# Kernel optimization log

Hardware: AMD Instinct MI355X
Metric: run time of the kernel (lower is better)

## Reference

```python
import jax, jax.numpy as jnp
import numpy as np

RADIUS = 4        # config.corr_radius
NUM_LEVELS = 4    # config.corr_levels
EPS = 1e-12       # F.normalize eps


def _avg_pool(x, s):
    # F.avg_pool2d(x, s, stride=s) for H,W divisible by s
    if s == 1:
        return x
    B, C, H, W = x.shape
    return x.reshape(B, C, H // s, s, W // s, s).mean(axis=(3, 5))


def _l2_normalize(x):
    # F.normalize(x, dim=1): x / max(||x||_2, eps)
    n = jnp.sqrt(jnp.sum(x * x, axis=1, keepdims=True))
    return x / jnp.maximum(n, EPS)


def _correlation(f1, f2, r=RADIUS):
    # windowed local correlation: corr[dy,dx](y,x) = sum_c f1(y,x) * f2(y-dy, x-dx)
    B, C, H, W = f1.shape
    f1 = _l2_normalize(f1)
    f2 = _l2_normalize(f2)
    f2p = jnp.pad(f2, ((0, 0), (0, 0), (r, r), (r, r)))  # zero pad = zero fill outside
    corrs = []
    for dy in range(-r, r + 1):
        for dx in range(-r, r + 1):
            sh = jax.lax.slice(f2p, (0, 0, r - dy, r - dx), (B, C, r - dy + H, r - dx + W))
            corrs.append(jnp.sum(f1 * sh, axis=1))  # [B,H,W]
    return jnp.stack(corrs, axis=1)  # [B, (2r+1)^2, H, W]


def setup_inputs() -> dict:
    key = jax.random.key(0)
    k1, k2, k3, k4 = jax.random.split(key, 4)
    B, C, H, W = 4, 256, 128, 192
    return {
        "fmap1": jax.random.normal(k1, (B, C, H, W), jnp.float32),
        "fmap2": jax.random.normal(k2, (B, C, H, W), jnp.float32),
        "depth1": jax.random.uniform(k3, (B, 1, H, W), jnp.float32),
        "depth2": jax.random.uniform(k4, (B, 1, H, W), jnp.float32),
        "depth_weight": jnp.asarray(0.1, jnp.float32),
    }


def reference(fmap1, fmap2, depth1, depth2, depth_weight):
    pyramid = []
    for i in range(NUM_LEVELS):
        s = 2 ** i
        corr = _correlation(_avg_pool(fmap1, s), _avg_pool(fmap2, s))
        # depth correlation enhancement: exp(-|d1 - d2|), broadcast over 81 channels
        dd = jnp.abs(_avg_pool(depth1, s) - _avg_pool(depth2, s))  # [B,1,h,w]
        corr = corr + depth_weight * jnp.exp(-dd)
        pyramid.append(corr)
    return tuple(pyramid)
```

## Files before the change

### kernel.cpp

```cpp
#include <hip/hip_runtime.h>
#include <hip/hip_bf16.h>

typedef __attribute__((ext_vector_type(8))) __bf16 bf16x8;
typedef __attribute__((ext_vector_type(4))) float f32x4;
typedef unsigned short ushort_t;
typedef unsigned int uint_t;

#define CCH 256
#define BB 4

#define NP32_0 3145728
#define NP32_1 786432
#define NP32_2 196608
#define NP32_3 49152

__device__ __forceinline__ ushort_t f2b(float v) {
    __hip_bfloat16 h = __float2bfloat16(v);
    return *reinterpret_cast<ushort_t*>(&h);
}

__device__ __forceinline__ void gload16(const void* g, void* l) {
    __builtin_amdgcn_global_load_lds(
        (const __attribute__((address_space(1))) void*)g,
        (__attribute__((address_space(3))) void*)l, 16, 0, 0);
}

struct PrepPtrs {
    ushort_t* o0; ushort_t* o1; ushort_t* o2; ushort_t* o3;
    float* n0; float* n1; float* n2; float* n3;
};

__global__ __launch_bounds__(256, 3) void pyr_prep_kernel(
    const float* __restrict__ fa, const float* __restrict__ fb,
    PrepPtrs Pa, PrepPtrs Pb)
{
    const int H = 128, W = 192;
    const int HW = H * W;
    const float* fin = blockIdx.y ? fb : fa;
    PrepPtrs P = blockIdx.y ? Pb : Pa;

    __shared__ float lds0[32 * 260];
    __shared__ float lds1[32 * 68];
    __shared__ float lds2[32 * 20];
    __shared__ float red[256];

    int xc = blockIdx.x % 6;
    int ys = (blockIdx.x / 6) % 16;
    int b  = blockIdx.x / 96;
    int gx0 = xc * 32, gy0 = ys * 8;
    int t = threadIdx.x;

    const float* gsrc[8];
    int lofs[8];
    #pragma unroll
    for (int j = 0; j < 8; ++j) {
        int e = t + 256 * j;
        int c = e >> 6, r = (e >> 3) & 7, x4 = e & 7;
        gsrc[j] = fin + ((size_t)(b * 256 + c) * H + gy0 + r) * W + gx0 + 4 * x4;
        lofs[j] = c * 260 + r * 32 + 4 * x4;
    }

    float4 stg[8];
    auto issue = [&](int kc) {
        #pragma unroll
        for (int j = 0; j < 8; ++j)
            stg[j] = *reinterpret_cast<const float4*>(gsrc[j] + (size_t)kc * (32 * HW));
    };

    float ssq0 = 0.f, ssq1 = 0.f, ssq2 = 0.f, ssq3 = 0.f;

    size_t p0g = (size_t)(b * H + gy0 + (t >> 5)) * W + gx0 + (t & 31);
    int wv = t >> 6, q = t & 63, qy = q >> 4, qx = q & 15;
    size_t l1g = (size_t)(b * 64 + ys * 4 + qy) * 96 + xc * 16 + qx;
    int cb2 = t >> 4, sI = t & 15, sy2 = sI >> 3, sx2 = sI & 7;
    size_t l2g = (size_t)(b * 32 + ys * 2 + sy2) * 48 + xc * 8 + sx2;
    int cb3 = t >> 2, u3 = t & 3;
    size_t l3g = (size_t)(b * 16 + ys) * 24 + xc * 4 + u3;

    issue(0);
    #pragma unroll 1
    for (int kc = 0; kc < 8; ++kc) {
        #pragma unroll
        for (int j = 0; j < 8; ++j)
            *reinterpret_cast<float4*>(&lds0[lofs[j]]) = stg[j];
        if (kc < 7) issue(kc + 1);
        __syncthreads();

        {
            uint_t uu[16];
            #pragma unroll
            for (int i = 0; i < 16; ++i) {
                float va = lds0[(2 * i) * 260 + t];
                float vb = lds0[(2 * i + 1) * 260 + t];
                ssq0 = fmaf(va, va, ssq0);
                ssq0 = fmaf(vb, vb, ssq0);
                uu[i] = (uint_t)f2b(va) | ((uint_t)f2b(vb) << 16);
            }
            ushort_t* dst = P.o0 + (size_t)kc * NP32_0 + p0g * 32;
            *reinterpret_cast<uint4*>(dst +  0) = make_uint4(uu[0],  uu[1],  uu[2],  uu[3]);
            *reinterpret_cast<uint4*>(dst +  8) = make_uint4(uu[4],  uu[5],  uu[6],  uu[7]);
            *reinterpret_cast<uint4*>(dst + 16) = make_uint4(uu[8],  uu[9],  uu[10], uu[11]);
            *reinterpret_cast<uint4*>(dst + 24) = make_uint4(uu[12], uu[13], uu[14], uu[15]);
        }

        {
            float a8[8];
            #pragma unroll
            for (int h = 0; h < 8; ++h) {
                int c = wv * 8 + h;
                float2 s0 = *reinterpret_cast<const float2*>(&lds0[c * 260 + (2 * qy) * 32 + 2 * qx]);
                float2 s1 = *reinterpret_cast<const float2*>(&lds0[c * 260 + (2 * qy + 1) * 32 + 2 * qx]);
                a8[h] = 0.25f * (s0.x + s0.y + s1.x + s1.y);
                ssq1 = fmaf(a8[h], a8[h], ssq1);
            }
            uint_t vv[4];
            #pragma unroll
            for (int i = 0; i < 4; ++i)
                vv[i] = (uint_t)f2b(a8[2 * i]) | ((uint_t)f2b(a8[2 * i + 1]) << 16);
            *reinterpret_cast<uint4*>(P.o1 + (size_t)kc * NP32_1 + l1g * 32 + wv * 8)
                = make_uint4(vv[0], vv[1], vv[2], vv[3]);
            #pragma unroll
            for (int h = 0; h < 8; ++h)
                lds1[(wv * 8 + h) * 68 + q] = a8[h];
        }
        __syncthreads();

        if (t < 128) {
            float a4[4];
            #pragma unroll
            for (int cc = 0; cc < 4; ++cc) {
                int c = cb2 * 4 + cc;
                float2 s0 = *reinterpret_cast<const float2*>(&lds1[c * 68 + (2 * sy2) * 16 + 2 * sx2]);
                float2 s1 = *reinterpret_cast<const float2*>(&lds1[c * 68 + (2 * sy2 + 1) * 16 + 2 * sx2]);
                a4[cc] = 0.25f * (s0.x + s0.y + s1.x + s1.y);
                ssq2 = fmaf(a4[cc], a4[cc], ssq2);
            }
            uint_t w0 = (uint_t)f2b(a4[0]) | ((uint_t)f2b(a4[1]) << 16);
            uint_t w1 = (uint_t)f2b(a4[2]) | ((uint_t)f2b(a4[3]) << 16);
            *reinterpret_cast<uint2*>(P.o2 + (size_t)kc * NP32_2 + l2g * 32 + cb2 * 4) = make_uint2(w0, w1);
            #pragma unroll
            for (int cc = 0; cc < 4; ++cc)
                lds2[(cb2 * 4 + cc) * 20 + sI] = a4[cc];
        }
        __syncthreads();

        if (t < 32) {
            float a4[4];
            #pragma unroll
            for (int cc = 0; cc < 4; ++cc) {
                int c = cb3 * 4 + cc;
                float2 s0 = *reinterpret_cast<const float2*>(&lds2[c * 20 + 2 * u3]);
                float2 s1 = *reinterpret_cast<const float2*>(&lds2[c * 20 + 8 + 2 * u3]);
                a4[cc] = 0.25f * (s0.x + s0.y + s1.x + s1.y);
                ssq3 = fmaf(a4[cc], a4[cc], ssq3);
            }
            uint_t w0 = (uint_t)f2b(a4[0]) | ((uint_t)f2b(a4[1]) << 16);
            uint_t w1 = (uint_t)f2b(a4[2]) | ((uint_t)f2b(a4[3]) << 16);
            *reinterpret_cast<uint2*>(P.o3 + (size_t)kc * NP32_3 + l3g * 32 + cb3 * 4) = make_uint2(w0, w1);
        }
    }

    P.n0[p0g] = 1.f / fmaxf(sqrtf(ssq0), 1e-12f);
    red[t] = ssq1;
    __syncthreads();
    if (t < 64) {
        float sm = red[t] + red[t + 64] + red[t + 128] + red[t + 192];
        P.n1[(size_t)(b * 64 + ys * 4 + (t >> 4)) * 96 + xc * 16 + (t & 15)]
            = 1.f / fmaxf(sqrtf(sm), 1e-12f);
    }
    __syncthreads();
    if (t < 128) red[t] = ssq2;
    __syncthreads();
    if (t < 16) {
        float sm = 0.f;
        #pragma unroll
        for (int c = 0; c < 8; ++c) sm += red[t + 16 * c];
        P.n2[(size_t)(b * 32 + ys * 2 + (t >> 3)) * 48 + xc * 8 + (t & 7)]
            = 1.f / fmaxf(sqrtf(sm), 1e-12f);
    }
    __syncthreads();
    if (t < 32) red[t] = ssq3;
    __syncthreads();
    if (t < 4) {
        float sm = 0.f;
        #pragma unroll
        for (int c = 0; c < 8; ++c) sm += red[t + 4 * c];
        P.n3[(size_t)(b * 16 + ys) * 24 + xc * 4 + t]
            = 1.f / fmaxf(sqrtf(sm), 1e-12f);
    }
}

struct CorrLvl {
    const ushort_t* f1n; const ushort_t* f2n;
    const float* in1; const float* in2; const float* dt;
    float* out;
    int H, W, TX, TY, npix32;
};

__global__ __launch_bounds__(256, 2) void corr_fused_kernel(
    CorrLvl Lv0, CorrLvl Lv1, CorrLvl Lv2, const ushort_t* __restrict__ zblk)
{
    __shared__ char smem[65536];
    char* As = smem;
    char* Bs = smem + 16384;

    int bid = blockIdx.x;
    CorrLvl L;
    int local;
    if (bid < 768)      { L = Lv0; local = bid; }
    else if (bid < 960) { L = Lv1; local = bid - 768; }
    else                { L = Lv2; local = bid - 960; }

    int H = L.H, W = L.W, TX = L.TX, TY = L.TY, npix32 = L.npix32;
    int cpx = (BB * TX * TY) >> 3;
    int swz = (local & 7) * cpx + (local >> 3);
    int tx = swz % TX;
    int ty = (swz / TX) % TY;
    int b  = swz / (TX * TY);
    int x0 = tx * 16, y0 = ty * 8;

    int tid = threadIdx.x;
    int w = tid >> 6, lane = tid & 63;
    int kg = lane >> 4, col = lane & 15;
    int r2 = col >> 2, c2 = col & 3;
    int sy = w >> 1, p = w & 1;
    int kgx = kg ^ c2;

    const ushort_t* srcA[2]; char* ldsA[2];
    #pragma unroll
    for (int q = 0; q < 2; ++q) {
        int row = w * 2 + q;
        int px = lane >> 2, js = lane & 3;
        int j = js ^ (px & 3);
        srcA[q] = L.f1n + ((size_t)((b * H + y0 + row) * W) + x0 + px) * 32 + j * 8;
        ldsA[q] = As + row * 1024;
    }
    const ushort_t* srcB[6]; int advB[6]; char* ldsB[6];
    #pragma unroll
    for (int q = 0; q < 6; ++q) {
        int u = (w * 6 + q) * 64 + lane;
        int row = u / 96, rem = u % 96;
        int px = rem >> 2, js = rem & 3;
        int j = js ^ (px & 3);
        int py = y0 - 4 + row, pxg = x0 - 4 + px;
        bool v = (py >= 0) && (py < H) && (pxg >= 0) && (pxg < W);
        srcB[q] = v ? (L.f2n + ((size_t)((b * H + py) * W) + pxg) * 32 + j * 8) : (zblk + j * 8);
        advB[q] = v ? npix32 : 0;
        ldsB[q] = Bs + (w * 6 + q) * 1024;
    }

    int aoff[2], boff[3][4];
    #pragma unroll
    for (int s = 0; s < 2; ++s) {
        int ly = 4 * sy + r2;
        int lx = 4 * (2 * p + s) + c2;
        aoff[s] = ((ly * 16 + lx) * 4 + kgx) * 16;
    }
    #pragma unroll
    for (int i = 0; i < 3; ++i)
        #pragma unroll
        for (int j = 0; j < 4; ++j) {
            int wy = 4 * (sy + i) + r2;
            int wx = 4 * (2 * p + j) + c2;
            boff[i][j] = ((wy * 24 + wx) * 4 + kgx) * 16;
        }

    f32x4 acc0[3][3] = {};
    f32x4 acc1[3][3] = {};

    #pragma unroll
    for (int q = 0; q < 2; ++q) { gload16(srcA[q], ldsA[q]); srcA[q] += npix32; }
    #pragma unroll
    for (int q = 0; q < 6; ++q) { gload16(srcB[q], ldsB[q]); srcB[q] += advB[q]; }

    int buf = 0;
    #pragma unroll 1
    for (int kc = 0; kc < 8; ++kc) {
        if (kc < 7) {
            int boA = (buf ^ 1) * 8192;
            int boB = (buf ^ 1) * 24576;
            #pragma unroll
            for (int q = 0; q < 2; ++q) { gload16(srcA[q], ldsA[q] + boA); srcA[q] += npix32; }
            #pragma unroll
            for (int q = 0; q < 6; ++q) { gload16(srcB[q], ldsB[q] + boB); srcB[q] += advB[q]; }
            __builtin_amdgcn_sched_barrier(0);
            asm volatile("s_waitcnt vmcnt(8)" ::: "memory");
        } else {
            __builtin_amdgcn_sched_barrier(0);
            asm volatile("s_waitcnt vmcnt(0)" ::: "memory");
        }
        __builtin_amdgcn_s_barrier();
        __builtin_amdgcn_sched_barrier(0);

        const char* Ab = As + buf * 8192;
        const char* Bb = Bs + buf * 24576;
        bf16x8 av0 = *(const bf16x8*)(Ab + aoff[0]);
        bf16x8 av1 = *(const bf16x8*)(Ab + aoff[1]);
        #pragma unroll
        for (int i = 0; i < 3; ++i) {
            #pragma unroll
            for (int j = 0; j < 4; ++j) {
                bf16x8 bv = *(const bf16x8*)(Bb + boff[i][j]);
                if (j < 3) acc0[i][j]     = __builtin_amdgcn_mfma_f32_16x16x32_bf16(av0, bv, acc0[i][j], 0, 0, 0);
                if (j > 0) acc1[i][j - 1] = __builtin_amdgcn_mfma_f32_16x16x32_bf16(av1, bv, acc1[i][j - 1], 0, 0, 0);
            }
        }
        if (kc < 7) {
            __builtin_amdgcn_sched_barrier(0);
            __builtin_amdgcn_s_barrier();
            __builtin_amdgcn_sched_barrier(0);
        }
        buf ^= 1;
    }

    float inv1v[2][4], dtv[2][4];
    #pragma unroll
    for (int s = 0; s < 2; ++s) {
        int sxs = 2 * p + s;
        #pragma unroll
        for (int rr = 0; rr < 4; ++rr) {
            int m = kg * 4 + rr;
            int iy = m >> 2, ix = m & 3;
            int pix = (b * H + y0 + 4 * sy + iy) * W + x0 + 4 * sxs + ix;
            inv1v[s][rr] = L.in1[pix];
            dtv[s][rr]   = L.dt[pix];
        }
    }
    #pragma unroll
    for (int s = 0; s < 2; ++s) {
        int sxs = 2 * p + s;
        #pragma unroll
        for (int i = 0; i < 3; ++i) {
            #pragma unroll
            for (int jj = 0; jj < 3; ++jj) {
                int wy = 4 * (sy + i) + r2;
                int wxr = 4 * (sxs + jj) + c2;
                int py = y0 - 4 + wy, px = x0 - 4 + wxr;
                bool v = (py >= 0) && (py < H) && (px >= 0) && (px < W);
                float i2 = v ? L.in2[(b * H + py) * W + px] : 0.f;
                f32x4 a = (s == 0) ? acc0[i][jj] : acc1[i][jj];
                #pragma unroll
                for (int rr = 0; rr < 4; ++rr) {
                    int m = kg * 4 + rr;
                    int iy = m >> 2, ix = m & 3;
                    int oy = iy + 8 - (4 * i + r2);
                    int ox = ix + 8 - (4 * jj + c2);
                    if (oy >= 0 && oy < 9 && ox >= 0 && ox < 9) {
                        int gy = y0 + 4 * sy + iy, gx = x0 + 4 * sxs + ix;
                        L.out[((size_t)(b * 81 + oy * 9 + ox) * H + gy) * W + gx]
                            = a[rr] * inv1v[s][rr] * i2 + dtv[s][rr];
                    }
                }
            }
        }
    }
}

__global__ __launch_bounds__(256) void corr_mfma_kernel(
    const ushort_t* __restrict__ f1n, const ushort_t* __restrict__ f2n,
    const float* __restrict__ invn1, const float* __restrict__ invn2,
    const float* __restrict__ dt, float* __restrict__ out,
    int H, int W, int TX, int TY, int zoff)
{
    int wid  = threadIdx.x >> 6;
    int lane = threadIdx.x & 63;
    int tile = blockIdx.x * 4 + wid;
    int ntiles = BB * TY * TX;
    if (tile >= ntiles) return;
    int tx = tile % TX;
    int ty = (tile / TX) % TY;
    int b  = tile / (TX * TY);
    int x0 = tx * 4, y0 = ty * 4;

    int col = lane & 15;
    int kg  = lane >> 4;

    int iyA = col >> 2, ixA = col & 3;
    int a_off = (((b * H + y0 + iyA) * W) + x0 + ixA) * 32 + kg * 8;

    int b_off[9], badv[9];
    uint_t vmask = 0;
    #pragma unroll
    for (int tt = 0; tt < 9; ++tt) {
        int w = tt * 16 + col;
        int wy = w / 12, wx = w % 12;
        int py = y0 + wy - 4, px = x0 + wx - 4;
        bool v = (py >= 0) && (py < H) && (px >= 0) && (px < W);
        b_off[tt] = v ? (((b * H + py) * W + px) * 32 + kg * 8) : (zoff + kg * 8);
        badv[tt] = v ? NP32_3 : 0;
        if (v) vmask |= (1u << tt);
    }

    f32x4 acc[9] = {};
    #pragma unroll
    for (int kb = 0; kb < 8; ++kb) {
        bf16x8 av = *reinterpret_cast<const bf16x8*>(f1n + a_off + kb * NP32_3);
        #pragma unroll
        for (int tt = 0; tt < 9; ++tt) {
            bf16x8 bv = *reinterpret_cast<const bf16x8*>(f2n + b_off[tt]);
            acc[tt] = __builtin_amdgcn_mfma_f32_16x16x32_bf16(av, bv, acc[tt], 0, 0, 0);
            b_off[tt] += badv[tt];
        }
    }

    float inv1[4], dts[4];
    #pragma unroll
    for (int r = 0; r < 4; ++r) {
        int m = kg * 4 + r;
        int iy = m >> 2, ix = m & 3;
        int pix = (b * H + y0 + iy) * W + x0 + ix;
        inv1[r] = invn1[pix];
        dts[r]  = dt[pix];
    }
    #pragma unroll
    for (int tt = 0; tt < 9; ++tt) {
        int w = tt * 16 + col;
        int wy = w / 12, wx = w % 12;
        int py = y0 + wy - 4, px = x0 + wx - 4;
        float i2 = ((vmask >> tt) & 1u) ? invn2[(b * H + py) * W + px] : 0.f;
        #pragma unroll
        for (int r = 0; r < 4; ++r) {
            int m = kg * 4 + r;
            int iy = m >> 2, ix = m & 3;
            int oy = iy + 8 - wy, ox = ix + 8 - wx;
            if (oy >= 0 && oy < 9 && ox >= 0 && ox < 9) {
                int o = oy * 9 + ox;
                out[((size_t)(b * 81 + o) * H + (y0 + iy)) * W + (x0 + ix)]
                    = acc[tt][r] * inv1[r] * i2 + dts[r];
            }
        }
    }
}

__global__ __launch_bounds__(256) void depth_kernel(
    const float* __restrict__ d1, const float* __restrict__ d2,
    const float* __restrict__ dw,
    float* __restrict__ dt0, float* __restrict__ dt1,
    float* __restrict__ dt2, float* __restrict__ dt3)
{
    int rid = blockIdx.x * 256 + threadIdx.x;
    if (rid >= 4 * 16 * 24) return;
    int b = rid / 384, rr = rid % 384, ry = rr / 24, rx = rr % 24;
    const int H = 128, W = 192;
    float w0 = dw[0];
    size_t base0 = ((size_t)b * H + ry * 8) * W + rx * 8;

    float q1[4][4], q2[4][4];
    #pragma unroll
    for (int yy = 0; yy < 4; ++yy) {
        float4 a0 = *reinterpret_cast<const float4*>(d1 + base0 + (2 * yy) * W);
        float4 a1 = *reinterpret_cast<const float4*>(d1 + base0 + (2 * yy) * W + 4);
        float4 a2 = *reinterpret_cast<const float4*>(d1 + base0 + (2 * yy + 1) * W);
        float4 a3 = *reinterpret_cast<const float4*>(d1 + base0 + (2 * yy + 1) * W + 4);
        float4 b0 = *reinterpret_cast<const float4*>(d2 + base0 + (2 * yy) * W);
        float4 b1 = *reinterpret_cast<const float4*>(d2 + base0 + (2 * yy) * W + 4);
        float4 b2 = *reinterpret_cast<const float4*>(d2 + base0 + (2 * yy + 1) * W);
        float4 b3 = *reinterpret_cast<const float4*>(d2 + base0 + (2 * yy + 1) * W + 4);
        float ra[2][8] = {{a0.x,a0.y,a0.z,a0.w,a1.x,a1.y,a1.z,a1.w},
                          {a2.x,a2.y,a2.z,a2.w,a3.x,a3.y,a3.z,a3.w}};
        float rb[2][8] = {{b0.x,b0.y,b0.z,b0.w,b1.x,b1.y,b1.z,b1.w},
                          {b2.x,b2.y,b2.z,b2.w,b3.x,b3.y,b3.z,b3.w}};
        #pragma unroll
        for (int e = 0; e < 2; ++e) {
            float o[8];
            #pragma unroll
            for (int xx = 0; xx < 8; ++xx) o[xx] = w0 * expf(-fabsf(ra[e][xx] - rb[e][xx]));
            *reinterpret_cast<float4*>(dt0 + base0 + (2 * yy + e) * W)     = make_float4(o[0], o[1], o[2], o[3]);
            *reinterpret_cast<float4*>(dt0 + base0 + (2 * yy + e) * W + 4) = make_float4(o[4], o[5], o[6], o[7]);
        }
        #pragma unroll
        for (int xx = 0; xx < 4; ++xx) {
            q1[yy][xx] = 0.25f * (ra[0][2 * xx] + ra[0][2 * xx + 1] + ra[1][2 * xx] + ra[1][2 * xx + 1]);
            q2[yy][xx] = 0.25f * (rb[0][2 * xx] + rb[0][2 * xx + 1] + rb[1][2 * xx] + rb[1][2 * xx + 1]);
        }
    }
    #pragma unroll
    for (int yy = 0; yy < 4; ++yy)
        #pragma unroll
        for (int xx = 0; xx < 4; ++xx)
            dt1[((size_t)b * 64 + ry * 4 + yy) * 96 + rx * 4 + xx] = w0 * expf(-fabsf(q1[yy][xx] - q2[yy][xx]));

    float r1[2][2], r2m[2][2];
    #pragma unroll
    for (int y = 0; y < 2; ++y)
        #pragma unroll
        for (int x = 0; x < 2; ++x) {
            r1[y][x]  = 0.25f * (q1[2 * y][2 * x] + q1[2 * y][2 * x + 1] + q1[2 * y + 1][2 * x] + q1[2 * y + 1][2 * x + 1]);
            r2m[y][x] = 0.25f * (q2[2 * y][2 * x] + q2[2 * y][2 * x + 1] + q2[2 * y + 1][2 * x] + q2[2 * y + 1][2 * x + 1]);
            dt2[((size_t)b * 32 + ry * 2 + y) * 48 + rx * 2 + x] = w0 * expf(-fabsf(r1[y][x] - r2m[y][x]));
        }
    float s1 = 0.25f * (r1[0][0] + r1[0][1] + r1[1][0] + r1[1][1]);
    float s2 = 0.25f * (r2m[0][0] + r2m[0][1] + r2m[1][0] + r2m[1][1]);
    dt3[((size_t)b * 16 + ry) * 24 + rx] = w0 * expf(-fabsf(s1 - s2));
}

extern "C" void kernel_launch(void* const* d_in, const int* in_sizes, int n_in,
                              void* d_out, int out_size, void* d_ws, size_t ws_size,
                              hipStream_t stream) {
    const float* f1 = (const float*)d_in[0];
    const float* f2 = (const float*)d_in[1];
    const float* d1 = (const float*)d_in[2];
    const float* d2 = (const float*)d_in[3];
    const float* dw = (const float*)d_in[4];
    float* out = (float*)d_out;
    float* ws  = (float*)d_ws;

    size_t o = 0;
    float* in1_0 = ws + o; o += (size_t)4 * 128 * 192;
    float* in1_1 = ws + o; o += (size_t)4 * 64 * 96;
    float* in1_2 = ws + o; o += (size_t)4 * 32 * 48;
    float* in1_3 = ws + o; o += (size_t)4 * 16 * 24;
    float* in2_0 = ws + o; o += (size_t)4 * 128 * 192;
    float* in2_1 = ws + o; o += (size_t)4 * 64 * 96;
    float* in2_2 = ws + o; o += (size_t)4 * 32 * 48;
    float* in2_3 = ws + o; o += (size_t)4 * 16 * 24;
    float* dt_0 = ws + o; o += (size_t)4 * 128 * 192;
    float* dt_1 = ws + o; o += (size_t)4 * 64 * 96;
    float* dt_2 = ws + o; o += (size_t)4 * 32 * 48;
    float* dt_3 = ws + o; o += (size_t)4 * 16 * 24;
    o = (o + 7) & ~(size_t)7;

    ushort_t* sws = (ushort_t*)(ws + o);
    const size_t L0 = (size_t)4 * 128 * 192 * 256;
    const size_t L1 = (size_t)4 * 64 * 96 * 256;
    const size_t L2 = (size_t)4 * 32 * 48 * 256;
    const size_t L3 = (size_t)4 * 16 * 24 * 256;
    const size_t FT = L0 + L1 + L2 + L3;
    ushort_t* f1n0 = sws;
    ushort_t* f1n1 = f1n0 + L0;
    ushort_t* f1n2 = f1n1 + L1;
    ushort_t* f1n3 = f1n2 + L2;
    ushort_t* f2n0 = sws + FT;
    ushort_t* f2n1 = f2n0 + L0;
    ushort_t* f2n2 = f2n1 + L1;
    ushort_t* f2n3 = f2n2 + L2;
    ushort_t* zblk = sws + 2 * FT;
    size_t need = o * 4 + (2 * FT + 256) * 2;
    if (ws_size < need) return;

    hipMemsetAsync(zblk, 0, 512, stream);

    depth_kernel<<<dim3(6), 256, 0, stream>>>(d1, d2, dw, dt_0, dt_1, dt_2, dt_3);

    PrepPtrs Pa = { f1n0, f1n1, f1n2, f1n3, in1_0, in1_1, in1_2, in1_3 };
    PrepPtrs Pb = { f2n0, f2n1, f2n2, f2n3, in2_0, in2_1, in2_2, in2_3 };
    pyr_prep_kernel<<<dim3(384, 2), 256, 0, stream>>>(f1, f2, Pa, Pb);

    CorrLvl lv0 = { f1n0, f2n0, in1_0, in2_0, dt_0, out,           128, 192, 12, 16, NP32_0 };
    CorrLvl lv1 = { f1n1, f2n1, in1_1, in2_1, dt_1, out + 7962624,  64,  96,  6,  8, NP32_1 };
    CorrLvl lv2 = { f1n2, f2n2, in1_2, in2_2, dt_2, out + 9953280,  32,  48,  3,  4, NP32_2 };
    corr_fused_kernel<<<dim3(1008), 256, 0, stream>>>(lv0, lv1, lv2, zblk);

    corr_mfma_kernel<<<dim3(96 / 4), 256, 0, stream>>>(f1n3, f2n3, in1_3, in2_3, dt_3, out + 10450944, 16, 24, 6, 4,
                                                       (int)(2 * FT - (size_t)(f2n3 - sws)));
}
```

Baseline: 241.2 us.

## Split pyramid prep into per-channel-chunk wave blocks with separate norm finalize

Replaces the LDS-staged prep kernel, whose 256-thread blocks loop over all 8 channel chunks, with single-wavefront blocks that each own one 32-channel chunk. The 2x2, 4x4 and 8x8 average pools are computed in registers with cross-lane shuffles instead of LDS and barriers. Partial sums of squares per chunk go to workspace, and a new small kernel adds the 8 partials and writes the inverse norms. This aims for more parallelism and fewer barriers, at the cost of an extra launch, more workspace traffic, and heavy register use from 112 packed words per thread.

```diff
diff --git a/kernel.cpp b/kernel.cpp
--- a/kernel.cpp
+++ b/kernel.cpp
@@ -14,6 +14,12 @@
 #define NP32_2 196608
 #define NP32_3 49152
 
+#define NPX0 98304
+#define NPX1 24576
+#define NPX2 6144
+#define NPX3 1536
+#define NPXT (NPX0 + NPX1 + NPX2 + NPX3)
+
 __device__ __forceinline__ ushort_t f2b(float v) {
     __hip_bfloat16 h = __float2bfloat16(v);
     return *reinterpret_cast<ushort_t*>(&h);
@@ -25,169 +31,146 @@
         (__attribute__((address_space(3))) void*)l, 16, 0, 0);
 }
 
-struct PrepPtrs {
+struct PrepOut {
     ushort_t* o0; ushort_t* o1; ushort_t* o2; ushort_t* o3;
+    float* s0; float* s1; float* s2; float* s3;
     float* n0; float* n1; float* n2; float* n3;
 };
 
-__global__ __launch_bounds__(256, 3) void pyr_prep_kernel(
+__global__ __launch_bounds__(64) void prep_stream_kernel(
     const float* __restrict__ fa, const float* __restrict__ fb,
-    PrepPtrs Pa, PrepPtrs Pb)
+    PrepOut Pa, PrepOut Pb)
 {
-    const int H = 128, W = 192;
-    const int HW = H * W;
+    const int H = 128, W = 192, HW = H * W;
     const float* fin = blockIdx.y ? fb : fa;
-    PrepPtrs P = blockIdx.y ? Pb : Pa;
-
-    __shared__ float lds0[32 * 260];
-    __shared__ float lds1[32 * 68];
-    __shared__ float lds2[32 * 20];
-    __shared__ float red[256];
-
-    int xc = blockIdx.x % 6;
-    int ys = (blockIdx.x / 6) % 16;
-    int b  = blockIdx.x / 96;
-    int gx0 = xc * 32, gy0 = ys * 8;
+    PrepOut P = blockIdx.y ? Pb : Pa;
+
+    int bid = blockIdx.x;
+    int kc = bid & 7;
+    int r0i = bid >> 3;
+    int xc = r0i % 12;
+    int ys = (r0i / 12) % 8;
+    int b  = r0i / 96;
+
     int t = threadIdx.x;
-
-    const float* gsrc[8];
-    int lofs[8];
-    #pragma unroll
-    for (int j = 0; j < 8; ++j) {
-        int e = t + 256 * j;
-        int c = e >> 6, r = (e >> 3) & 7, x4 = e & 7;
-        gsrc[j] = fin + ((size_t)(b * 256 + c) * H + gy0 + r) * W + gx0 + 4 * x4;
-        lofs[j] = c * 260 + r * 32 + 4 * x4;
-    }
-
-    float4 stg[8];
-    auto issue = [&](int kc) {
-        #pragma unroll
-        for (int j = 0; j < 8; ++j)
-            stg[j] = *reinterpret_cast<const float4*>(gsrc[j] + (size_t)kc * (32 * HW));
-    };
-
-    float ssq0 = 0.f, ssq1 = 0.f, ssq2 = 0.f, ssq3 = 0.f;
-
-    size_t p0g = (size_t)(b * H + gy0 + (t >> 5)) * W + gx0 + (t & 31);
-    int wv = t >> 6, q = t & 63, qy = q >> 4, qx = q & 15;
-    size_t l1g = (size_t)(b * 64 + ys * 4 + qy) * 96 + xc * 16 + qx;
-    int cb2 = t >> 4, sI = t & 15, sy2 = sI >> 3, sx2 = sI & 7;
-    size_t l2g = (size_t)(b * 32 + ys * 2 + sy2) * 48 + xc * 8 + sx2;
-    int cb3 = t >> 2, u3 = t & 3;
-    size_t l3g = (size_t)(b * 16 + ys) * 24 + xc * 4 + u3;
-
-    issue(0);
-    #pragma unroll 1
-    for (int kc = 0; kc < 8; ++kc) {
-        #pragma unroll
-        for (int j = 0; j < 8; ++j)
-            *reinterpret_cast<float4*>(&lds0[lofs[j]]) = stg[j];
-        if (kc < 7) issue(kc + 1);
-        __syncthreads();
-
-        {
-            uint_t uu[16];
-            #pragma unroll
-            for (int i = 0; i < 16; ++i) {
-                float va = lds0[(2 * i) * 260 + t];
-                float vb = lds0[(2 * i + 1) * 260 + t];
-                ssq0 = fmaf(va, va, ssq0);
-                ssq0 = fmaf(vb, vb, ssq0);
-                uu[i] = (uint_t)f2b(va) | ((uint_t)f2b(vb) << 16);
-            }
-            ushort_t* dst = P.o0 + (size_t)kc * NP32_0 + p0g * 32;
-            *reinterpret_cast<uint4*>(dst +  0) = make_uint4(uu[0],  uu[1],  uu[2],  uu[3]);
-            *reinterpret_cast<uint4*>(dst +  8) = make_uint4(uu[4],  uu[5],  uu[6],  uu[7]);
-            *reinterpret_cast<uint4*>(dst + 16) = make_uint4(uu[8],  uu[9],  uu[10], uu[11]);
-            *reinterpret_cast<uint4*>(dst + 24) = make_uint4(uu[12], uu[13], uu[14], uu[15]);
-        }
-
-        {
-            float a8[8];
-            #pragma unroll
-            for (int h = 0; h < 8; ++h) {
-                int c = wv * 8 + h;
-                float2 s0 = *reinterpret_cast<const float2*>(&lds0[c * 260 + (2 * qy) * 32 + 2 * qx]);
-                float2 s1 = *reinterpret_cast<const float2*>(&lds0[c * 260 + (2 * qy + 1) * 32 + 2 * qx]);
-                a8[h] = 0.25f * (s0.x + s0.y + s1.x + s1.y);
-                ssq1 = fmaf(a8[h], a8[h], ssq1);
-            }
-            uint_t vv[4];
-            #pragma unroll
-            for (int i = 0; i < 4; ++i)
-                vv[i] = (uint_t)f2b(a8[2 * i]) | ((uint_t)f2b(a8[2 * i + 1]) << 16);
-            *reinterpret_cast<uint4*>(P.o1 + (size_t)kc * NP32_1 + l1g * 32 + wv * 8)
-                = make_uint4(vv[0], vv[1], vv[2], vv[3]);
-            #pragma unroll
-            for (int h = 0; h < 8; ++h)
-                lds1[(wv * 8 + h) * 68 + q] = a8[h];
-        }
-        __syncthreads();
-
-        if (t < 128) {
-            float a4[4];
-            #pragma unroll
-            for (int cc = 0; cc < 4; ++cc) {
-                int c = cb2 * 4 + cc;
-                float2 s0 = *reinterpret_cast<const float2*>(&lds1[c * 68 + (2 * sy2) * 16 + 2 * sx2]);
-                float2 s1 = *reinterpret_cast<const float2*>(&lds1[c * 68 + (2 * sy2 + 1) * 16 + 2 * sx2]);
-                a4[cc] = 0.25f * (s0.x + s0.y + s1.x + s1.y);
-                ssq2 = fmaf(a4[cc], a4[cc], ssq2);
-            }
-            uint_t w0 = (uint_t)f2b(a4[0]) | ((uint_t)f2b(a4[1]) << 16);
-            uint_t w1 = (uint_t)f2b(a4[2]) | ((uint_t)f2b(a4[3]) << 16);
-            *reinterpret_cast<uint2*>(P.o2 + (size_t)kc * NP32_2 + l2g * 32 + cb2 * 4) = make_uint2(w0, w1);
-            #pragma unroll
-            for (int cc = 0; cc < 4; ++cc)
-                lds2[(cb2 * 4 + cc) * 20 + sI] = a4[cc];
-        }
-        __syncthreads();
-
-        if (t < 32) {
-            float a4[4];
-            #pragma unroll
-            for (int cc = 0; cc < 4; ++cc) {
-                int c = cb3 * 4 + cc;
-                float2 s0 = *reinterpret_cast<const float2*>(&lds2[c * 20 + 2 * u3]);
-                float2 s1 = *reinterpret_cast<const float2*>(&lds2[c * 20 + 8 + 2 * u3]);
-                a4[cc] = 0.25f * (s0.x + s0.y + s1.x + s1.y);
-                ssq3 = fmaf(a4[cc], a4[cc], ssq3);
-            }
-            uint_t w0 = (uint_t)f2b(a4[0]) | ((uint_t)f2b(a4[1]) << 16);
-            uint_t w1 = (uint_t)f2b(a4[2]) | ((uint_t)f2b(a4[3]) << 16);
-            *reinterpret_cast<uint2*>(P.o3 + (size_t)kc * NP32_3 + l3g * 32 + cb3 * 4) = make_uint2(w0, w1);
-        }
-    }
-
-    P.n0[p0g] = 1.f / fmaxf(sqrtf(ssq0), 1e-12f);
-    red[t] = ssq1;
-    __syncthreads();
-    if (t < 64) {
-        float sm = red[t] + red[t + 64] + red[t + 128] + red[t + 192];
-        P.n1[(size_t)(b * 64 + ys * 4 + (t >> 4)) * 96 + xc * 16 + (t & 15)]
-            = 1.f / fmaxf(sqrtf(sm), 1e-12f);
-    }
-    __syncthreads();
-    if (t < 128) red[t] = ssq2;
-    __syncthreads();
-    if (t < 16) {
-        float sm = 0.f;
-        #pragma unroll
-        for (int c = 0; c < 8; ++c) sm += red[t + 16 * c];
-        P.n2[(size_t)(b * 32 + ys * 2 + (t >> 3)) * 48 + xc * 8 + (t & 7)]
-            = 1.f / fmaxf(sqrtf(sm), 1e-12f);
-    }
-    __syncthreads();
-    if (t < 32) red[t] = ssq3;
-    __syncthreads();
-    if (t < 4) {
-        float sm = 0.f;
-        #pragma unroll
-        for (int c = 0; c < 8; ++c) sm += red[t + 4 * c];
-        P.n3[(size_t)(b * 16 + ys) * 24 + xc * 4 + t]
-            = 1.f / fmaxf(sqrtf(sm), 1e-12f);
-    }
+    int ty = t >> 3, tx = t & 7;
+    int row0 = ys * 16 + 2 * ty;
+    int col0 = xc * 16 + 2 * tx;
+
+    const float* base = fin + (size_t)(b * 256 + kc * 32) * HW + (size_t)row0 * W + col0;
+
+    uint_t uu0[4][16];
+    uint_t uu1[16], uu2[16], uu3[16];
+    float sq0 = 0.f, sq1v = 0.f, sq2v = 0.f, sq3v = 0.f;
+    float ssqA = 0.f, ssqB = 0.f, ssqC = 0.f, ssqD = 0.f;
+    float ssq1 = 0.f, ssq2 = 0.f, ssq3 = 0.f;
+    (void)sq0; (void)sq1v; (void)sq2v; (void)sq3v;
+
+    bool own2 = ((tx & 1) | (ty & 1)) == 0;
+    bool own3 = ((tx & 3) | (ty & 3)) == 0;
+
+    #pragma unroll
+    for (int cc = 0; cc < 32; ++cc) {
+        float2 ra = *reinterpret_cast<const float2*>(base + (size_t)cc * HW);
+        float2 rb = *reinterpret_cast<const float2*>(base + (size_t)cc * HW + W);
+
+        ssqA = fmaf(ra.x, ra.x, ssqA);
+        ssqB = fmaf(ra.y, ra.y, ssqB);
+        ssqC = fmaf(rb.x, rb.x, ssqC);
+        ssqD = fmaf(rb.y, rb.y, ssqD);
+
+        ushort_t b00 = f2b(ra.x), b01 = f2b(ra.y), b10 = f2b(rb.x), b11 = f2b(rb.y);
+        if ((cc & 1) == 0) {
+            uu0[0][cc >> 1] = (uint_t)b00;
+            uu0[1][cc >> 1] = (uint_t)b01;
+            uu0[2][cc >> 1] = (uint_t)b10;
+            uu0[3][cc >> 1] = (uint_t)b11;
+        } else {
+            uu0[0][cc >> 1] |= ((uint_t)b00) << 16;
+            uu0[1][cc >> 1] |= ((uint_t)b01) << 16;
+            uu0[2][cc >> 1] |= ((uint_t)b10) << 16;
+            uu0[3][cc >> 1] |= ((uint_t)b11) << 16;
+        }
+
+        float l1 = 0.25f * (ra.x + ra.y + rb.x + rb.y);
+        ssq1 = fmaf(l1, l1, ssq1);
+        if ((cc & 1) == 0) uu1[cc >> 1] = (uint_t)f2b(l1);
+        else               uu1[cc >> 1] |= ((uint_t)f2b(l1)) << 16;
+
+        float sa = l1 + __shfl_xor(l1, 1);
+        float l2 = 0.25f * (sa + __shfl_xor(sa, 8));
+        float sb = l2 + __shfl_xor(l2, 2);
+        float l3 = 0.25f * (sb + __shfl_xor(sb, 16));
+
+        if (own2) ssq2 = fmaf(l2, l2, ssq2);
+        if (own3) ssq3 = fmaf(l3, l3, ssq3);
+        if ((cc & 1) == 0) { uu2[cc >> 1] = (uint_t)f2b(l2); uu3[cc >> 1] = (uint_t)f2b(l3); }
+        else               { uu2[cc >> 1] |= ((uint_t)f2b(l2)) << 16; uu3[cc >> 1] |= ((uint_t)f2b(l3)) << 16; }
+    }
+
+    float sqv[4] = { ssqA, ssqB, ssqC, ssqD };
+    #pragma unroll
+    for (int r = 0; r < 2; ++r)
+        #pragma unroll
+        for (int cx = 0; cx < 2; ++cx) {
+            int pxi = r * 2 + cx;
+            size_t px = (size_t)(b * H + row0 + r) * W + col0 + cx;
+            ushort_t* dst = P.o0 + (size_t)kc * NP32_0 + px * 32;
+            *reinterpret_cast<uint4*>(dst +  0) = make_uint4(uu0[pxi][0],  uu0[pxi][1],  uu0[pxi][2],  uu0[pxi][3]);
+            *reinterpret_cast<uint4*>(dst +  8) = make_uint4(uu0[pxi][4],  uu0[pxi][5],  uu0[pxi][6],  uu0[pxi][7]);
+            *reinterpret_cast<uint4*>(dst + 16) = make_uint4(uu0[pxi][8],  uu0[pxi][9],  uu0[pxi][10], uu0[pxi][11]);
+            *reinterpret_cast<uint4*>(dst + 24) = make_uint4(uu0[pxi][12], uu0[pxi][13], uu0[pxi][14], uu0[pxi][15]);
+            P.s0[(size_t)kc * NPX0 + px] = sqv[pxi];
+        }
+
+    size_t l1px = (size_t)(b * 64 + ys * 8 + ty) * 96 + xc * 8 + tx;
+    {
+        ushort_t* dst = P.o1 + (size_t)kc * NP32_1 + l1px * 32;
+        *reinterpret_cast<uint4*>(dst +  0) = make_uint4(uu1[0],  uu1[1],  uu1[2],  uu1[3]);
+        *reinterpret_cast<uint4*>(dst +  8) = make_uint4(uu1[4],  uu1[5],  uu1[6],  uu1[7]);
+        *reinterpret_cast<uint4*>(dst + 16) = make_uint4(uu1[8],  uu1[9],  uu1[10], uu1[11]);
+        *reinterpret_cast<uint4*>(dst + 24) = make_uint4(uu1[12], uu1[13], uu1[14], uu1[15]);
+        P.s1[(size_t)kc * NPX1 + l1px] = ssq1;
+    }
+
+    if (own2) {
+        size_t l2px = (size_t)(b * 32 + ys * 4 + (ty >> 1)) * 48 + xc * 4 + (tx >> 1);
+        ushort_t* dst = P.o2 + (size_t)kc * NP32_2 + l2px * 32;
+        *reinterpret_cast<uint4*>(dst +  0) = make_uint4(uu2[0],  uu2[1],  uu2[2],  uu2[3]);
+        *reinterpret_cast<uint4*>(dst +  8) = make_uint4(uu2[4],  uu2[5],  uu2[6],  uu2[7]);
+        *reinterpret_cast<uint4*>(dst + 16) = make_uint4(uu2[8],  uu2[9],  uu2[10], uu2[11]);
+        *reinterpret_cast<uint4*>(dst + 24) = make_uint4(uu2[12], uu2[13], uu2[14], uu2[15]);
+        P.s2[(size_t)kc * NPX2 + l2px] = ssq2;
+    }
+
+    if (own3) {
+        size_t l3px = (size_t)(b * 16 + ys * 2 + (ty >> 2)) * 24 + xc * 2 + (tx >> 2);
+        ushort_t* dst = P.o3 + (size_t)kc * NP32_3 + l3px * 32;
+        *reinterpret_cast<uint4*>(dst +  0) = make_uint4(uu3[0],  uu3[1],  uu3[2],  uu3[3]);
+        *reinterpret_cast<uint4*>(dst +  8) = make_uint4(uu3[4],  uu3[5],  uu3[6],  uu3[7]);
+        *reinterpret_cast<uint4*>(dst + 16) = make_uint4(uu3[8],  uu3[9],  uu3[10], uu3[11]);
+        *reinterpret_cast<uint4*>(dst + 24) = make_uint4(uu3[12], uu3[13], uu3[14], uu3[15]);
+        P.s3[(size_t)kc * NPX3 + l3px] = ssq3;
+    }
+}
+
+__global__ __launch_bounds__(256) void invnorm_fin_kernel(PrepOut Pa, PrepOut Pb)
+{
+    int tid = blockIdx.x * 256 + threadIdx.x;
+    if (tid >= 2 * NPXT) return;
+    PrepOut P = (tid >= NPXT) ? Pb : Pa;
+    int i = (tid >= NPXT) ? (tid - NPXT) : tid;
+
+    const float* s; float* n; int npx, j;
+    if (i < NPX0)                       { s = P.s0; n = P.n0; npx = NPX0; j = i; }
+    else if (i < NPX0 + NPX1)           { s = P.s1; n = P.n1; npx = NPX1; j = i - NPX0; }
+    else if (i < NPX0 + NPX1 + NPX2)    { s = P.s2; n = P.n2; npx = NPX2; j = i - NPX0 - NPX1; }
+    else                                { s = P.s3; n = P.n3; npx = NPX3; j = i - NPX0 - NPX1 - NPX2; }
+
+    float sum = 0.f;
+    #pragma unroll
+    for (int k = 0; k < 8; ++k) sum += s[(size_t)k * npx + j];
+    n[j] = 1.f / fmaxf(sqrtf(sum), 1e-12f);
 }
 
 struct CorrLvl {
@@ -506,25 +489,33 @@
     float* ws  = (float*)d_ws;
 
     size_t o = 0;
-    float* in1_0 = ws + o; o += (size_t)4 * 128 * 192;
-    float* in1_1 = ws + o; o += (size_t)4 * 64 * 96;
-    float* in1_2 = ws + o; o += (size_t)4 * 32 * 48;
-    float* in1_3 = ws + o; o += (size_t)4 * 16 * 24;
-    float* in2_0 = ws + o; o += (size_t)4 * 128 * 192;
-    float* in2_1 = ws + o; o += (size_t)4 * 64 * 96;
-    float* in2_2 = ws + o; o += (size_t)4 * 32 * 48;
-    float* in2_3 = ws + o; o += (size_t)4 * 16 * 24;
-    float* dt_0 = ws + o; o += (size_t)4 * 128 * 192;
-    float* dt_1 = ws + o; o += (size_t)4 * 64 * 96;
-    float* dt_2 = ws + o; o += (size_t)4 * 32 * 48;
-    float* dt_3 = ws + o; o += (size_t)4 * 16 * 24;
+    float* in1_0 = ws + o; o += NPX0;
+    float* in1_1 = ws + o; o += NPX1;
+    float* in1_2 = ws + o; o += NPX2;
+    float* in1_3 = ws + o; o += NPX3;
+    float* in2_0 = ws + o; o += NPX0;
+    float* in2_1 = ws + o; o += NPX1;
+    float* in2_2 = ws + o; o += NPX2;
+    float* in2_3 = ws + o; o += NPX3;
+    float* dt_0 = ws + o; o += NPX0;
+    float* dt_1 = ws + o; o += NPX1;
+    float* dt_2 = ws + o; o += NPX2;
+    float* dt_3 = ws + o; o += NPX3;
+    float* s1_0 = ws + o; o += (size_t)8 * NPX0;
+    float* s1_1 = ws + o; o += (size_t)8 * NPX1;
+    float* s1_2 = ws + o; o += (size_t)8 * NPX2;
+    float* s1_3 = ws + o; o += (size_t)8 * NPX3;
+    float* s2_0 = ws + o; o += (size_t)8 * NPX0;
+    float* s2_1 = ws + o; o += (size_t)8 * NPX1;
+    float* s2_2 = ws + o; o += (size_t)8 * NPX2;
+    float* s2_3 = ws + o; o += (size_t)8 * NPX3;
     o = (o + 7) & ~(size_t)7;
 
     ushort_t* sws = (ushort_t*)(ws + o);
-    const size_t L0 = (size_t)4 * 128 * 192 * 256;
-    const size_t L1 = (size_t)4 * 64 * 96 * 256;
-    const size_t L2 = (size_t)4 * 32 * 48 * 256;
-    const size_t L3 = (size_t)4 * 16 * 24 * 256;
+    const size_t L0 = (size_t)NPX0 * 256;
+    const size_t L1 = (size_t)NPX1 * 256;
+    const size_t L2 = (size_t)NPX2 * 256;
+    const size_t L3 = (size_t)NPX3 * 256;
     const size_t FT = L0 + L1 + L2 + L3;
     ushort_t* f1n0 = sws;
     ushort_t* f1n1 = f1n0 + L0;
@@ -542,9 +533,11 @@
 
     depth_kernel<<<dim3(6), 256, 0, stream>>>(d1, d2, dw, dt_0, dt_1, dt_2, dt_3);
 
-    PrepPtrs Pa = { f1n0, f1n1, f1n2, f1n3, in1_0, in1_1, in1_2, in1_3 };
-    PrepPtrs Pb = { f2n0, f2n1, f2n2, f2n3, in2_0, in2_1, in2_2, in2_3 };
-    pyr_prep_kernel<<<dim3(384, 2), 256, 0, stream>>>(f1, f2, Pa, Pb);
+    PrepOut Pa = { f1n0, f1n1, f1n2, f1n3, s1_0, s1_1, s1_2, s1_3, in1_0, in1_1, in1_2, in1_3 };
+    PrepOut Pb = { f2n0, f2n1, f2n2, f2n3, s2_0, s2_1, s2_2, s2_3, in2_0, in2_1, in2_2, in2_3 };
+
+    prep_stream_kernel<<<dim3(3072, 2), 64, 0, stream>>>(f1, f2, Pa, Pb);
+    invnorm_fin_kernel<<<dim3((2 * NPXT + 255) / 256), 256, 0, stream>>>(Pa, Pb);
 
     CorrLvl lv0 = { f1n0, f2n0, in1_0, in2_0, dt_0, out,           128, 192, 12, 16, NP32_0 };
     CorrLvl lv1 = { f1n1, f2n1, in1_1, in2_1, dt_1, out + 7962624,  64,  96,  6,  8, NP32_1 };
```

Result: no change. 240.4 us (-0.3%).
